# Kernel optimization log

Measured on AMD Instinct MI355X. Metric: run time of the kernel, lower is better.

The kernel has to match this reference:

```python
import jax, jax.numpy as jnp
import numpy as np

N_NODES = 4096
N_EDGES = 131072
C_IN = 256
C_OUT = 256
N_HEADS = 4
ALPHA = 0.2
NEG_FILL = -9e15


def setup_inputs() -> dict:
    key = jax.random.key(0)
    k_x, k_e, k_w, k_b, k_a = jax.random.split(key, 5)
    x = jax.random.normal(k_x, (N_NODES, C_IN), dtype=jnp.float32)
    edge_index = jax.random.randint(k_e, (2, N_EDGES), 0, N_NODES, dtype=jnp.int64)
    # nn.Linear(c_in, c_out): weight [c_out, c_in], bias [c_out]
    W = jax.random.normal(k_w, (C_OUT, C_IN), dtype=jnp.float32) * 0.05
    b = jax.random.normal(k_b, (C_OUT,), dtype=jnp.float32) * 0.05
    # attention vector a: [num_heads, 2 * c_out_per_head]
    a = jax.random.normal(k_a, (N_HEADS, 2 * (C_OUT // N_HEADS)), dtype=jnp.float32) * 0.05
    return {"x": x, "edge_index": edge_index, "W": W, "b": b, "a": a}


def reference(x, edge_index, W, b, a):
    N = x.shape[0]
    H = a.shape[0]
    C = W.shape[0] // H  # per-head feature dim

    # Linear projection then split heads: [N, H, C]
    feats = (x @ W.T + b).reshape(N, H, C)

    # Dense adjacency (faithful to the original index_select/scatter construction)
    adj = jnp.zeros((N, N), dtype=bool).at[edge_index[0], edge_index[1]].set(True)

    # attn_logits = leaky_relu(einsum('bhc,hc->bh', cat(f_i, f_j), a))
    # is separable: score(i,j,h) = leaky_relu(f_i . a[:, :C] + f_j . a[:, C:])
    s_src = jnp.einsum('nhc,hc->nh', feats, a[:, :C])  # [N, H]
    s_dst = jnp.einsum('nhc,hc->nh', feats, a[:, C:])  # [N, H]
    logits = jax.nn.leaky_relu(s_src[:, None, :] + s_dst[None, :, :], ALPHA)  # [N, N, H]

    masked = jnp.where(adj[..., None], logits, NEG_FILL)
    probs = jax.nn.softmax(masked, axis=1)  # softmax over source nodes j (dim=2 with batch)

    # Weighted aggregation: einsum('bijh,bjhc->bihc') then concat heads
    out = jnp.einsum('ijh,jhc->ihc', probs, feats).reshape(N, H * C)
    return out[None]  # [1, N, c_out] (batch_size = 1 in the original)
```

## Files before the change

### kernel.cpp

```cpp
#include <hip/hip_runtime.h>
#include <hip/hip_bf16.h>
#include <stdint.h>

#define N_NODES 4096
#define N_EDGES 131072
#define C_IN 256
#define C_OUT 256
#define N_HEADS 4
#define C_HEAD 64
#define MAX_DEG 128

typedef __attribute__((ext_vector_type(8))) short short8;
typedef __attribute__((ext_vector_type(4))) float floatx4;

__device__ __forceinline__ short f2bf(float f) {
    __hip_bfloat16 h = __float2bfloat16(f);
    return *reinterpret_cast<short*>(&h);
}

__global__ void detect_dtype(const uint32_t* __restrict__ xw, int* __restrict__ flag) {
    if (threadIdx.x == 0 && blockIdx.x == 0) {
        int hits = 0;
        for (int q = 0; q < 64; ++q) {
            uint32_t e = ((xw[q] & 0xFFFFu) >> 7) & 0xFFu;
            if (e >= 96u && e <= 144u) ++hits;
        }
        *flag = (hits >= 32) ? 0 : 1;
    }
}

__global__ void scatter_edges(const int* __restrict__ ei,
                              unsigned short* __restrict__ nbr,
                              int* __restrict__ deg) {
    int e = blockIdx.x * blockDim.x + threadIdx.x;
    if (e >= N_EDGES) return;
    bool is64 = true;
    #pragma unroll
    for (int q = 1; q < 64; q += 2) is64 = is64 && (ei[q] == 0);
    int row, col;
    if (is64) {
        const long long* e64 = (const long long*)ei;
        row = (int)e64[e];
        col = (int)e64[N_EDGES + e];
    } else {
        row = ei[e];
        col = ei[N_EDGES + e];
    }
    int pos = atomicAdd(&deg[row], 1);
    if (pos < MAX_DEG) nbr[row * MAX_DEG + pos] = (unsigned short)col;
}

__global__ __launch_bounds__(256) void gemm_feats(
    const void* __restrict__ xv, const void* __restrict__ Wv,
    const void* __restrict__ bv, const int* __restrict__ flag,
    __hip_bfloat16* __restrict__ feats)
{
    int f32 = *flag;
    int tid  = threadIdx.x;
    int lane = tid & 63;
    int wave = tid >> 6;
    int tile = blockIdx.x * 4 + wave;
    int row0 = (tile >> 4) * 16;
    int col0 = (tile & 15) * 16;
    int r    = lane & 15;
    int quad = lane >> 4;

    floatx4 acc = {0.f, 0.f, 0.f, 0.f};
    if (f32) {
        const floatx4* ax = (const floatx4*)((const float*)xv + (size_t)(row0 + r) * C_IN);
        const floatx4* bw = (const floatx4*)((const float*)Wv + (size_t)(col0 + r) * C_IN);
        #pragma unroll
        for (int k8 = 0; k8 < 8; ++k8) {
            floatx4 a0 = ax[k8 * 8 + quad * 2], a1 = ax[k8 * 8 + quad * 2 + 1];
            floatx4 b0 = bw[k8 * 8 + quad * 2], b1 = bw[k8 * 8 + quad * 2 + 1];
            short8 av, bq;
            #pragma unroll
            for (int j = 0; j < 4; ++j) {
                av[j] = f2bf(a0[j]); av[4 + j] = f2bf(a1[j]);
                bq[j] = f2bf(b0[j]); bq[4 + j] = f2bf(b1[j]);
            }
            acc = __builtin_amdgcn_mfma_f32_16x16x32_bf16(av, bq, acc, 0, 0, 0);
        }
    } else {
        const short8* ax = (const short8*)((const __hip_bfloat16*)xv + (size_t)(row0 + r) * C_IN);
        const short8* bw = (const short8*)((const __hip_bfloat16*)Wv + (size_t)(col0 + r) * C_IN);
        #pragma unroll
        for (int k8 = 0; k8 < 8; ++k8) {
            short8 av = ax[k8 * 4 + quad];
            short8 bq = bw[k8 * 4 + quad];
            acc = __builtin_amdgcn_mfma_f32_16x16x32_bf16(av, bq, acc, 0, 0, 0);
        }
    }

    int gn = col0 + r;
    float bias = f32 ? ((const float*)bv)[gn]
                     : __bfloat162float(((const __hip_bfloat16*)bv)[gn]);
    #pragma unroll
    for (int rr = 0; rr < 4; ++rr) {
        int gm = row0 + quad * 4 + rr;
        feats[(size_t)gm * C_OUT + gn] = __float2bfloat16(acc[rr] + bias);
    }
}

__global__ void score_kernel(const __hip_bfloat16* __restrict__ feats,
                             const void* __restrict__ av_in,
                             const int* __restrict__ flag,
                             float* __restrict__ s_src,
                             float* __restrict__ s_dst)
{
    int f32 = *flag;
    int gid = blockIdx.x * blockDim.x + threadIdx.x;
    if (gid >= N_NODES * N_HEADS) return;
    int n = gid >> 2, h = gid & 3;
    const __hip_bfloat16* f = feats + (size_t)n * C_OUT + h * C_HEAD;
    float ss = 0.f, sd = 0.f;
    if (f32) {
        const float* a0 = (const float*)av_in + h * 2 * C_HEAD;
        #pragma unroll 8
        for (int c = 0; c < C_HEAD; ++c) {
            float fv = __bfloat162float(f[c]);
            ss += fv * a0[c];
            sd += fv * a0[C_HEAD + c];
        }
    } else {
        const __hip_bfloat16* a0 = (const __hip_bfloat16*)av_in + h * 2 * C_HEAD;
        #pragma unroll 8
        for (int c = 0; c < C_HEAD; ++c) {
            float fv = __bfloat162float(f[c]);
            ss += fv * __bfloat162float(a0[c]);
            sd += fv * __bfloat162float(a0[C_HEAD + c]);
        }
    }
    s_src[gid] = ss;
    s_dst[gid] = sd;
}

__global__ __launch_bounds__(256) void aggregate(
    const unsigned short* __restrict__ nbr,
    const int* __restrict__ deg,
    const __hip_bfloat16* __restrict__ feats,
    const float* __restrict__ s_src,
    const float* __restrict__ s_dst,
    float* __restrict__ out)
{
    int i = blockIdx.x;
    int t = threadIdx.x;
    int h = t >> 6;

    __shared__ unsigned short lst[MAX_DEG];
    __shared__ unsigned char  ok[MAX_DEG];
    __shared__ float wk[MAX_DEG * N_HEADS];

    int n = deg[i];
    n = (n < MAX_DEG) ? n : MAX_DEG;

    if (t < n) lst[t] = nbr[i * MAX_DEG + t];
    __syncthreads();
    if (t < n) {
        unsigned short v = lst[t];
        bool keep = true;
        for (int q = 0; q < t; ++q) keep = keep && (lst[q] != v);
        ok[t] = keep ? 1 : 0;
    }
    __syncthreads();
    for (int p = t; p < n * N_HEADS; p += 256) {
        int k = p >> 2, hh = p & 3;
        float l = s_src[i * N_HEADS + hh] + s_dst[(int)lst[k] * N_HEADS + hh];
        l = (l > 0.f) ? l : 0.2f * l;
        l = fminf(fmaxf(l, -60.f), 60.f);
        wk[k * N_HEADS + hh] = ok[k] ? __expf(l) : 0.f;
    }
    __syncthreads();

    float acc = 0.f, denom = 0.f;
    if (n > 0) {
        for (int k = 0; k < n; ++k) {
            float w = wk[k * N_HEADS + h];
            denom += w;
            acc += w * __bfloat162float(feats[(size_t)lst[k] * C_OUT + t]);
        }
        if (denom <= 0.f) denom = 1.f;
    } else {
        for (int j = 0; j < N_NODES; ++j)
            acc += __bfloat162float(feats[(size_t)j * C_OUT + t]);
        denom = (float)N_NODES;
    }
    out[(size_t)i * C_OUT + t] = acc / denom;
}

extern "C" void kernel_launch(void* const* d_in, const int* in_sizes, int n_in,
                              void* d_out, int out_size, void* d_ws, size_t ws_size,
                              hipStream_t stream) {
    const void* x  = d_in[0];
    const int*  ei = (const int*)d_in[1];
    const void* W  = d_in[2];
    const void* b  = d_in[3];
    const void* a  = d_in[4];
    float* out = (float*)d_out;

    uint8_t* ws = (uint8_t*)d_ws;
    __hip_bfloat16* feats = (__hip_bfloat16*)ws;
    unsigned short* nbr   = (unsigned short*)(ws + (2u << 20));
    int*            deg   = (int*)(ws + (3u << 20));
    float*          s_src = (float*)(ws + (3u << 20) + (16u << 10));
    float*          s_dst = (float*)(ws + (3u << 20) + (80u << 10));
    int*            flag  = (int*)(ws + (3u << 20) + (144u << 10));

    hipMemsetAsync(deg, 0, N_NODES * sizeof(int), stream);
    detect_dtype<<<1, 64, 0, stream>>>((const uint32_t*)x, flag);
    scatter_edges<<<N_EDGES / 256, 256, 0, stream>>>(ei, nbr, deg);
    gemm_feats<<<(N_NODES / 16) * (C_OUT / 16) / 4, 256, 0, stream>>>(x, W, b, flag, feats);
    score_kernel<<<N_NODES * N_HEADS / 256, 256, 0, stream>>>(feats, a, flag, s_src, s_dst);
    aggregate<<<N_NODES, 256, 0, stream>>>(nbr, deg, feats, s_src, s_dst, out);
}
```

Before: 118.7 us.

## Drop dtype detection, vectorize score kernel, split aggregate neighbors across waves

Removes the runtime dtype-detection kernel and its flag, hard-coding fp32 inputs so one launch and the per-kernel branches disappear. The score kernel now reads features as 8-wide bf16 vectors and the attention vector as float4. The aggregate kernel splits neighbors across four waves, each lane loading four bf16 features at once, then combines the partial sums through shared memory and writes float4 results. This trades a dependent serial neighbor loop for extra LDS reduction and a serial denominator sum in wave 0.

```diff
diff --git a/kernel.cpp b/kernel.cpp
--- a/kernel.cpp
+++ b/kernel.cpp
@@ -11,22 +11,16 @@
 #define MAX_DEG 128
 
 typedef __attribute__((ext_vector_type(8))) short short8;
+typedef __attribute__((ext_vector_type(4))) short short4v;
 typedef __attribute__((ext_vector_type(4))) float floatx4;
 
+union f32u { float f; uint32_t u; };
+__device__ __forceinline__ float bf2f(short s) {
+    f32u v; v.u = ((uint32_t)(uint16_t)s) << 16; return v.f;
+}
 __device__ __forceinline__ short f2bf(float f) {
     __hip_bfloat16 h = __float2bfloat16(f);
     return *reinterpret_cast<short*>(&h);
-}
-
-__global__ void detect_dtype(const uint32_t* __restrict__ xw, int* __restrict__ flag) {
-    if (threadIdx.x == 0 && blockIdx.x == 0) {
-        int hits = 0;
-        for (int q = 0; q < 64; ++q) {
-            uint32_t e = ((xw[q] & 0xFFFFu) >> 7) & 0xFFu;
-            if (e >= 96u && e <= 144u) ++hits;
-        }
-        *flag = (hits >= 32) ? 0 : 1;
-    }
 }
 
 __global__ void scatter_edges(const int* __restrict__ ei,
@@ -51,11 +45,9 @@
 }
 
 __global__ __launch_bounds__(256) void gemm_feats(
-    const void* __restrict__ xv, const void* __restrict__ Wv,
-    const void* __restrict__ bv, const int* __restrict__ flag,
-    __hip_bfloat16* __restrict__ feats)
+    const float* __restrict__ x, const float* __restrict__ W,
+    const float* __restrict__ b, __hip_bfloat16* __restrict__ feats)
 {
-    int f32 = *flag;
     int tid  = threadIdx.x;
     int lane = tid & 63;
     int wave = tid >> 6;
@@ -65,36 +57,25 @@
     int r    = lane & 15;
     int quad = lane >> 4;
 
+    const floatx4* ax = (const floatx4*)(x + (size_t)(row0 + r) * C_IN);
+    const floatx4* bw = (const floatx4*)(W + (size_t)(col0 + r) * C_IN);
+
     floatx4 acc = {0.f, 0.f, 0.f, 0.f};
-    if (f32) {
-        const floatx4* ax = (const floatx4*)((const float*)xv + (size_t)(row0 + r) * C_IN);
-        const floatx4* bw = (const floatx4*)((const float*)Wv + (size_t)(col0 + r) * C_IN);
+    #pragma unroll
+    for (int k8 = 0; k8 < 8; ++k8) {
+        floatx4 a0 = ax[k8 * 8 + quad * 2], a1 = ax[k8 * 8 + quad * 2 + 1];
+        floatx4 b0 = bw[k8 * 8 + quad * 2], b1 = bw[k8 * 8 + quad * 2 + 1];
+        short8 av, bq;
         #pragma unroll
-        for (int k8 = 0; k8 < 8; ++k8) {
-            floatx4 a0 = ax[k8 * 8 + quad * 2], a1 = ax[k8 * 8 + quad * 2 + 1];
-            floatx4 b0 = bw[k8 * 8 + quad * 2], b1 = bw[k8 * 8 + quad * 2 + 1];
-            short8 av, bq;
-            #pragma unroll
-            for (int j = 0; j < 4; ++j) {
-                av[j] = f2bf(a0[j]); av[4 + j] = f2bf(a1[j]);
-                bq[j] = f2bf(b0[j]); bq[4 + j] = f2bf(b1[j]);
-            }
-            acc = __builtin_amdgcn_mfma_f32_16x16x32_bf16(av, bq, acc, 0, 0, 0);
-        }
-    } else {
-        const short8* ax = (const short8*)((const __hip_bfloat16*)xv + (size_t)(row0 + r) * C_IN);
-        const short8* bw = (const short8*)((const __hip_bfloat16*)Wv + (size_t)(col0 + r) * C_IN);
-        #pragma unroll
-        for (int k8 = 0; k8 < 8; ++k8) {
-            short8 av = ax[k8 * 4 + quad];
-            short8 bq = bw[k8 * 4 + quad];
-            acc = __builtin_amdgcn_mfma_f32_16x16x32_bf16(av, bq, acc, 0, 0, 0);
-        }
+        for (int j = 0; j < 4; ++j) {
+            av[j] = f2bf(a0[j]); av[4 + j] = f2bf(a1[j]);
+            bq[j] = f2bf(b0[j]); bq[4 + j] = f2bf(b1[j]);
+        }
+        acc = __builtin_amdgcn_mfma_f32_16x16x32_bf16(av, bq, acc, 0, 0, 0);
     }
 
     int gn = col0 + r;
-    float bias = f32 ? ((const float*)bv)[gn]
-                     : __bfloat162float(((const __hip_bfloat16*)bv)[gn]);
+    float bias = b[gn];
     #pragma unroll
     for (int rr = 0; rr < 4; ++rr) {
         int gm = row0 + quad * 4 + rr;
@@ -102,33 +83,26 @@
     }
 }
 
-__global__ void score_kernel(const __hip_bfloat16* __restrict__ feats,
-                             const void* __restrict__ av_in,
-                             const int* __restrict__ flag,
-                             float* __restrict__ s_src,
-                             float* __restrict__ s_dst)
+__global__ __launch_bounds__(64) void score_kernel(
+    const __hip_bfloat16* __restrict__ feats, const float* __restrict__ a,
+    float* __restrict__ s_src, float* __restrict__ s_dst)
 {
-    int f32 = *flag;
-    int gid = blockIdx.x * blockDim.x + threadIdx.x;
-    if (gid >= N_NODES * N_HEADS) return;
+    int gid = blockIdx.x * 64 + threadIdx.x;
     int n = gid >> 2, h = gid & 3;
-    const __hip_bfloat16* f = feats + (size_t)n * C_OUT + h * C_HEAD;
+    const short8*  f  = (const short8*)(feats + (size_t)n * C_OUT + h * C_HEAD);
+    const floatx4* as = (const floatx4*)(a + h * 2 * C_HEAD);
     float ss = 0.f, sd = 0.f;
-    if (f32) {
-        const float* a0 = (const float*)av_in + h * 2 * C_HEAD;
-        #pragma unroll 8
-        for (int c = 0; c < C_HEAD; ++c) {
-            float fv = __bfloat162float(f[c]);
-            ss += fv * a0[c];
-            sd += fv * a0[C_HEAD + c];
-        }
-    } else {
-        const __hip_bfloat16* a0 = (const __hip_bfloat16*)av_in + h * 2 * C_HEAD;
-        #pragma unroll 8
-        for (int c = 0; c < C_HEAD; ++c) {
-            float fv = __bfloat162float(f[c]);
-            ss += fv * __bfloat162float(a0[c]);
-            sd += fv * __bfloat162float(a0[C_HEAD + c]);
+    #pragma unroll
+    for (int v = 0; v < 8; ++v) {
+        short8 fv = f[v];
+        floatx4 s0 = as[v * 2],      s1 = as[v * 2 + 1];
+        floatx4 d0 = as[16 + v * 2], d1 = as[16 + v * 2 + 1];
+        #pragma unroll
+        for (int j = 0; j < 4; ++j) {
+            float x0 = bf2f(fv[j]);
+            float x1 = bf2f(fv[4 + j]);
+            ss += x0 * s0[j] + x1 * s1[j];
+            sd += x0 * d0[j] + x1 * d1[j];
         }
     }
     s_src[gid] = ss;
@@ -143,13 +117,16 @@
     const float* __restrict__ s_dst,
     float* __restrict__ out)
 {
-    int i = blockIdx.x;
-    int t = threadIdx.x;
-    int h = t >> 6;
+    int i    = blockIdx.x;
+    int t    = threadIdx.x;
+    int wv   = t >> 6;
+    int lane = t & 63;
+    int h    = lane >> 4;
 
     __shared__ unsigned short lst[MAX_DEG];
     __shared__ unsigned char  ok[MAX_DEG];
-    __shared__ float wk[MAX_DEG * N_HEADS];
+    __shared__ float          wk[MAX_DEG][N_HEADS];
+    __shared__ floatx4        red[4][64];
 
     int n = deg[i];
     n = (n < MAX_DEG) ? n : MAX_DEG;
@@ -167,35 +144,61 @@
         int k = p >> 2, hh = p & 3;
         float l = s_src[i * N_HEADS + hh] + s_dst[(int)lst[k] * N_HEADS + hh];
         l = (l > 0.f) ? l : 0.2f * l;
-        l = fminf(fmaxf(l, -60.f), 60.f);
-        wk[k * N_HEADS + hh] = ok[k] ? __expf(l) : 0.f;
-    }
-    __syncthreads();
-
-    float acc = 0.f, denom = 0.f;
+        l = fminf(l, 60.f);
+        wk[k][hh] = ok[k] ? __expf(l) : 0.f;
+    }
+    __syncthreads();
+
+    floatx4 acc = {0.f, 0.f, 0.f, 0.f};
     if (n > 0) {
-        for (int k = 0; k < n; ++k) {
-            float w = wk[k * N_HEADS + h];
-            denom += w;
-            acc += w * __bfloat162float(feats[(size_t)lst[k] * C_OUT + t]);
-        }
-        if (denom <= 0.f) denom = 1.f;
+        for (int k = wv; k < n; k += 4) {
+            float w = wk[k][h];
+            short4v fv = *(const short4v*)(feats + (size_t)lst[k] * C_OUT + lane * 4);
+            acc[0] += w * bf2f(fv[0]);
+            acc[1] += w * bf2f(fv[1]);
+            acc[2] += w * bf2f(fv[2]);
+            acc[3] += w * bf2f(fv[3]);
+        }
     } else {
-        for (int j = 0; j < N_NODES; ++j)
-            acc += __bfloat162float(feats[(size_t)j * C_OUT + t]);
-        denom = (float)N_NODES;
-    }
-    out[(size_t)i * C_OUT + t] = acc / denom;
+        for (int j = wv; j < N_NODES; j += 4) {
+            short4v fv = *(const short4v*)(feats + (size_t)j * C_OUT + lane * 4);
+            acc[0] += bf2f(fv[0]);
+            acc[1] += bf2f(fv[1]);
+            acc[2] += bf2f(fv[2]);
+            acc[3] += bf2f(fv[3]);
+        }
+    }
+    red[wv][lane] = acc;
+    __syncthreads();
+
+    if (wv == 0) {
+        floatx4 r0 = red[0][lane], r1 = red[1][lane], r2 = red[2][lane], r3 = red[3][lane];
+        float denom;
+        if (n > 0) {
+            denom = 0.f;
+            for (int k = 0; k < n; ++k) denom += wk[k][h];
+            if (denom <= 0.f) denom = 1.f;
+        } else {
+            denom = (float)N_NODES;
+        }
+        float inv = 1.0f / denom;
+        floatx4 o;
+        o[0] = (r0[0] + r1[0] + r2[0] + r3[0]) * inv;
+        o[1] = (r0[1] + r1[1] + r2[1] + r3[1]) * inv;
+        o[2] = (r0[2] + r1[2] + r2[2] + r3[2]) * inv;
+        o[3] = (r0[3] + r1[3] + r2[3] + r3[3]) * inv;
+        *(floatx4*)(out + (size_t)i * C_OUT + lane * 4) = o;
+    }
 }
 
 extern "C" void kernel_launch(void* const* d_in, const int* in_sizes, int n_in,
                               void* d_out, int out_size, void* d_ws, size_t ws_size,
                               hipStream_t stream) {
-    const void* x  = d_in[0];
-    const int*  ei = (const int*)d_in[1];
-    const void* W  = d_in[2];
-    const void* b  = d_in[3];
-    const void* a  = d_in[4];
+    const float* x  = (const float*)d_in[0];
+    const int*   ei = (const int*)d_in[1];
+    const float* W  = (const float*)d_in[2];
+    const float* b  = (const float*)d_in[3];
+    const float* a  = (const float*)d_in[4];
     float* out = (float*)d_out;
 
     uint8_t* ws = (uint8_t*)d_ws;
@@ -204,12 +207,10 @@
     int*            deg   = (int*)(ws + (3u << 20));
     float*          s_src = (float*)(ws + (3u << 20) + (16u << 10));
     float*          s_dst = (float*)(ws + (3u << 20) + (80u << 10));
-    int*            flag  = (int*)(ws + (3u << 20) + (144u << 10));
 
     hipMemsetAsync(deg, 0, N_NODES * sizeof(int), stream);
-    detect_dtype<<<1, 64, 0, stream>>>((const uint32_t*)x, flag);
     scatter_edges<<<N_EDGES / 256, 256, 0, stream>>>(ei, nbr, deg);
-    gemm_feats<<<(N_NODES / 16) * (C_OUT / 16) / 4, 256, 0, stream>>>(x, W, b, flag, feats);
-    score_kernel<<<N_NODES * N_HEADS / 256, 256, 0, stream>>>(feats, a, flag, s_src, s_dst);
+    gemm_feats<<<(N_NODES / 16) * (C_OUT / 16) / 4, 256, 0, stream>>>(x, W, b, feats);
+    score_kernel<<<N_NODES * N_HEADS / 64, 64, 0, stream>>>(feats, a, s_src, s_dst);
     aggregate<<<N_NODES, 256, 0, stream>>>(nbr, deg, feats, s_src, s_dst, out);
 }
```

Result: faster. 111.2 us (-6.3%).
